# Optimization experiments

Hardware: AMD Instinct MI355X
Metric: run time of the kernel (lower is better)

## Reference

```python
import jax, jax.numpy as jnp
import numpy as np

N_NODES = 50000
N_EDGES = 500000
HIDDEN = 128
N_REL = 8


def setup_inputs() -> dict:
    key = jax.random.key(0)
    ks = jax.random.split(key, 6)
    node_states = jax.random.normal(ks[0], (N_NODES, HIDDEN), dtype=jnp.float32)
    edge_index = jax.random.randint(ks[1], (2, N_EDGES), 0, N_NODES, dtype=jnp.int64)
    edge_type = jax.random.randint(ks[2], (N_EDGES,), 0, N_REL, dtype=jnp.int64)
    # nn.Linear params: weight [out, in], applied as x @ W.T (+ b)
    W_self = jax.random.normal(ks[3], (HIDDEN, HIDDEN), dtype=jnp.float32) / np.sqrt(HIDDEN)
    b_self = jax.random.normal(ks[4], (HIDDEN,), dtype=jnp.float32) * 0.01
    W_rel = jax.random.normal(ks[5], (N_REL, HIDDEN, HIDDEN), dtype=jnp.float32) / np.sqrt(HIDDEN)
    return {"node_states": node_states, "edge_index": edge_index, "edge_type": edge_type,
            "W_self": W_self, "b_self": b_self, "W_rel": W_rel}


def reference(node_states, edge_index, edge_type, W_self, b_self, W_rel):
    # Per-relation gather -> linear -> scatter-add, with mean (degree) normalization.
    # Dropout is identity (eval mode).
    n_nodes = node_states.shape[0]
    n_rel = W_rel.shape[0]
    src = edge_index[0]
    dst = edge_index[1]
    xs = node_states[src]                                  # [E, d] gather once
    # Select per-edge relation transform without materializing [E, R, d]:
    # fixed small loop over relations, masked accumulate.
    messages = jnp.zeros_like(xs)
    for r in range(n_rel):
        m_r = xs @ W_rel[r].T                              # [E, d]
        messages = messages + jnp.where((edge_type == r)[:, None], m_r, 0.0)
    agg = jax.ops.segment_sum(messages, dst, num_segments=n_nodes)          # [N, d]
    deg = jax.ops.segment_sum(jnp.ones((dst.shape[0], 1), node_states.dtype),
                              dst, num_segments=n_nodes)                    # [N, 1]
    agg = agg / jnp.maximum(deg, 1.0)
    out = jax.nn.relu(node_states @ W_self.T + b_self + agg)
    return out
```

## Files before the change

kernel.cpp:

```cpp
#include <hip/hip_runtime.h>

#define HIDDEN 128
#define N_REL 8
#define ZCOLS 1152
#define BK 32
#define CPAD 136

typedef short short8 __attribute__((ext_vector_type(8)));
typedef float f32x4 __attribute__((ext_vector_type(4)));

__device__ inline float dot4f(float4 a, float4 b) {
  return a.x*b.x + a.y*b.y + a.z*b.z + a.w*b.w;
}

__device__ inline unsigned short f32_to_bf16(float f) {
  unsigned u = __float_as_uint(f);
  unsigned r = (u + 0x7FFFu + ((u >> 16) & 1u)) >> 16;
  return (unsigned short)r;
}

__device__ inline float bf16_to_f32(unsigned short h) {
  return __uint_as_float(((unsigned)h) << 16);
}

__device__ inline void gload_lds16(const unsigned short* g, unsigned short* l) {
  __builtin_amdgcn_global_load_lds(
      (const __attribute__((address_space(1))) void*)g,
      (__attribute__((address_space(3))) void*)l, 16, 0, 0);
}

__global__ void zero_i(int* __restrict__ p, int n) {
  int i = blockIdx.x * blockDim.x + threadIdx.x;
  int stride = gridDim.x * blockDim.x;
  for (; i < n; i += stride) p[i] = 0;
}

__global__ void hist_dst(const int* __restrict__ ei, int E, int* __restrict__ deg) {
  int i = blockIdx.x * blockDim.x + threadIdx.x;
  int stride = gridDim.x * blockDim.x;
  for (int e = i; e < E; e += stride) atomicAdd(&deg[ei[E + e]], 1);
}

__global__ void scan_pass1(const int* __restrict__ deg, int N, int N1,
                           int* __restrict__ rs, int* __restrict__ bsum) {
  __shared__ int sh[256];
  int tid = threadIdx.x;
  int i = blockIdx.x * 256 + tid;
  int v = (i < N) ? deg[i] : 0;
  sh[tid] = v;
  __syncthreads();
  for (int off = 1; off < 256; off <<= 1) {
    int x = (tid >= off) ? sh[tid - off] : 0;
    __syncthreads();
    sh[tid] += x;
    __syncthreads();
  }
  if (i < N1) rs[i] = sh[tid] - v;
  if (tid == 255) bsum[blockIdx.x] = sh[255];
}

__global__ void scan_pass2(int* __restrict__ bsum, int nb) {
  __shared__ int sh[256];
  int tid = threadIdx.x;
  int v = (tid < nb) ? bsum[tid] : 0;
  sh[tid] = v;
  __syncthreads();
  for (int off = 1; off < 256; off <<= 1) {
    int x = (tid >= off) ? sh[tid - off] : 0;
    __syncthreads();
    sh[tid] += x;
    __syncthreads();
  }
  if (tid < nb) bsum[tid] = sh[tid] - v;
}

__global__ void scan_pass3(int* __restrict__ rs, const int* __restrict__ bsum,
                           int* __restrict__ cursor, int N, int N1) {
  int i = blockIdx.x * 256 + threadIdx.x;
  if (i < N1) {
    int v = rs[i] + bsum[blockIdx.x];
    rs[i] = v;
    if (i < N) cursor[i] = v;
  }
}

__global__ void scatter_sorted(const int* __restrict__ ei, const int* __restrict__ et,
                               int E, int* __restrict__ cursor, int* __restrict__ sorted) {
  int i = blockIdx.x * blockDim.x + threadIdx.x;
  int stride = gridDim.x * blockDim.x;
  for (int e = i; e < E; e += stride) {
    int d = ei[E + e];
    int pos = atomicAdd(&cursor[d], 1);
    sorted[pos] = ei[e] | (et[e] << 24);
  }
}


__global__ void convert_xw(const float* __restrict__ ns,
                           const float* __restrict__ Ws, const float* __restrict__ Wr,
                           unsigned short* __restrict__ Xb,
                           unsigned short* __restrict__ Wb, int N) {
  int totalX = N * (HIDDEN / 8);
  int totalW = ZCOLS * (HIDDEN / 8);
  int i = blockIdx.x * blockDim.x + threadIdx.x;
  int stride = gridDim.x * blockDim.x;
  for (; i < totalX + totalW; i += stride) {
    const float* src;
    unsigned short* dst;
    if (i < totalX) {
      int row = i >> 4;
      int off = (i & 15) * 8;
      src = ns + (size_t)row * HIDDEN + off;
      dst = Xb + (size_t)row * HIDDEN + off;
    } else {
      int w = i - totalX;
      int j = w >> 4;
      int k = (w & 15) * 8;
      src = (j < HIDDEN) ? Ws + (size_t)j * HIDDEN + k
                         : Wr + (size_t)(j - HIDDEN) * HIDDEN + k;
      dst = Wb + (size_t)j * HIDDEN + k;
    }
    float4 a = *(const float4*)src, b = *(const float4*)(src + 4);
    ushort4 h0, h1;
    h0.x = f32_to_bf16(a.x); h0.y = f32_to_bf16(a.y);
    h0.z = f32_to_bf16(a.z); h0.w = f32_to_bf16(a.w);
    h1.x = f32_to_bf16(b.x); h1.y = f32_to_bf16(b.y);
    h1.z = f32_to_bf16(b.z); h1.w = f32_to_bf16(b.w);
    *(ushort4*)dst = h0;
    *(ushort4*)(dst + 4) = h1;
  }
}

__global__ __launch_bounds__(256) void gemm_z(
    const unsigned short* __restrict__ Xb, const unsigned short* __restrict__ Wb,
    unsigned short* __restrict__ Z, int N)
{
  __shared__ __align__(16) char smem[128 * CPAD * 2];
  unsigned short (*As)[128][BK] = (unsigned short (*)[128][BK])smem;
  unsigned short (*Bs)[128][BK] = (unsigned short (*)[128][BK])(smem + 16384);
  unsigned short (*Ct)[CPAD]    = (unsigned short (*)[CPAD])smem;

  int nwg = (int)gridDim.x;
  int orig = blockIdx.x;
  int q = nwg >> 3, r = nwg & 7;
  int xcd = orig & 7, off = orig >> 3;
  int bid = (xcd < r ? xcd * (q + 1) : r * (q + 1) + (xcd - r) * q) + off;

  int t = threadIdx.x;
  int lane = t & 63;
  int wave = t >> 6;
  int colb = lane & 15;
  int kq = (lane >> 4) * 8;
  int wr = (wave >> 1) * 64;
  int wc = (wave & 1) * 64;
  int rowbase = (bid / (ZCOLS / 128)) * 128;
  int colbase = (bid % (ZCOLS / 128)) * 128;

  int srow0 = t >> 2,         sk = (t & 3) * 8;
  int srow1 = (256 + t) >> 2;

  int ga0 = rowbase + srow0; if (ga0 >= N) ga0 = N - 1;
  int ga1 = rowbase + srow1; if (ga1 >= N) ga1 = N - 1;
  int gb0 = colbase + srow0; if (gb0 >= ZCOLS) gb0 = ZCOLS - 1;
  int gb1 = colbase + srow1; if (gb1 >= ZCOLS) gb1 = ZCOLS - 1;

  f32x4 acc[4][4];
  #pragma unroll
  for (int m = 0; m < 4; ++m)
    #pragma unroll
    for (int n = 0; n < 4; ++n) acc[m][n] = (f32x4){0.f, 0.f, 0.f, 0.f};

  gload_lds16(Xb + (size_t)ga0 * HIDDEN + sk, &As[0][srow0][sk]);
  gload_lds16(Xb + (size_t)ga1 * HIDDEN + sk, &As[0][srow1][sk]);
  gload_lds16(Wb + (size_t)gb0 * HIDDEN + sk, &Bs[0][srow0][sk]);
  gload_lds16(Wb + (size_t)gb1 * HIDDEN + sk, &Bs[0][srow1][sk]);
  __syncthreads();

  int cur = 0;
  for (int ks = 0; ks < 4; ++ks) {
    if (ks < 3) {
      int k0 = (ks + 1) * BK;
      gload_lds16(Xb + (size_t)ga0 * HIDDEN + k0 + sk, &As[cur ^ 1][srow0][sk]);
      gload_lds16(Xb + (size_t)ga1 * HIDDEN + k0 + sk, &As[cur ^ 1][srow1][sk]);
      gload_lds16(Wb + (size_t)gb0 * HIDDEN + k0 + sk, &Bs[cur ^ 1][srow0][sk]);
      gload_lds16(Wb + (size_t)gb1 * HIDDEN + k0 + sk, &Bs[cur ^ 1][srow1][sk]);
    }

    short8 a[4], bb[4];
    #pragma unroll
    for (int m = 0; m < 4; ++m)
      a[m] = *(const short8*)&As[cur][wr + m * 16 + colb][kq];
    #pragma unroll
    for (int n = 0; n < 4; ++n)
      bb[n] = *(const short8*)&Bs[cur][wc + n * 16 + colb][kq];

    #pragma unroll
    for (int m = 0; m < 4; ++m)
      #pragma unroll
      for (int n = 0; n < 4; ++n)
        acc[m][n] = __builtin_amdgcn_mfma_f32_16x16x32_bf16(a[m], bb[n],
                                                            acc[m][n], 0, 0, 0);
    if (ks < 3) {
      __syncthreads();
      cur ^= 1;
    }
  }

  __syncthreads();
  #pragma unroll
  for (int m = 0; m < 4; ++m) {
    int row = wr + m * 16 + (lane >> 4) * 4;
    #pragma unroll
    for (int n = 0; n < 4; ++n) {
      int c = wc + n * 16 + colb;
      #pragma unroll
      for (int rr = 0; rr < 4; ++rr)
        Ct[row + rr][c] = f32_to_bf16(acc[m][n][rr]);
    }
  }
  __syncthreads();

  int rowt = t >> 4;
  int ck = (t & 15) * 8;
  for (int p = 0; p < 8; ++p) {
    int row = p * 16 + rowt;
    int gr = rowbase + row;
    if (gr < N) {
      short8 v = *(const short8*)&Ct[row][ck];
      *(short8*)(Z + (size_t)gr * ZCOLS + colbase + ck) = v;
    }
  }
}

__global__ __launch_bounds__(256) void gather_out(
    const unsigned short* __restrict__ Z, const int* __restrict__ sorted,
    const int* __restrict__ rs, const float* __restrict__ b,
    float* __restrict__ out, int N)
{
  int wid = (int)((blockIdx.x * (unsigned)blockDim.x + threadIdx.x) >> 6);
  int lane = threadIdx.x & 63;
  if (wid >= N) return;
  int s0 = rs[wid], s1 = rs[wid + 1];

  int g = lane >> 3;
  int cl = lane & 7;

  float acc[16];
  #pragma unroll
  for (int k = 0; k < 16; ++k) acc[k] = 0.f;

  for (int eb = s0; eb < s1; eb += 64) {
    int m = min(64, s1 - eb);
    int sv = (lane < m) ? sorted[eb + lane] : 0;
    for (int j = 0; j < m; j += 8) {
      int e = j + g;
      int pk = __shfl(sv, e);
      if (e < m) {
        int src = pk & 0x00FFFFFF;
        if (src >= N) src = 0;
        int sl = (pk >> 24) & 7;
        const unsigned short* base = Z + (size_t)src * ZCOLS + HIDDEN + sl * HIDDEN;
        short8 v0 = *(const short8*)(base + cl * 8);
        short8 v1 = *(const short8*)(base + 64 + cl * 8);
        #pragma unroll
        for (int k = 0; k < 8; ++k) {
          acc[k]     += bf16_to_f32((unsigned short)v0[k]);
          acc[8 + k] += bf16_to_f32((unsigned short)v1[k]);
        }
      }
    }
  }

  #pragma unroll
  for (int k = 0; k < 16; ++k) {
    acc[k] += __shfl_xor(acc[k], 32);
    acc[k] += __shfl_xor(acc[k], 16);
    acc[k] += __shfl_xor(acc[k], 8);
  }

  if (g == 0) {
    float inv = (s1 > s0) ? 1.0f / (float)(s1 - s0) : 0.0f;
    const unsigned short* zp = Z + (size_t)wid * ZCOLS;
    short8 zv0 = *(const short8*)(zp + cl * 8);
    short8 zv1 = *(const short8*)(zp + 64 + cl * 8);
    float* op = out + (size_t)wid * HIDDEN;
    #pragma unroll
    for (int h = 0; h < 2; ++h) {
      const short8& zv = h ? zv1 : zv0;
      int cbase = h * 64 + cl * 8;
      float4 b0 = *(const float4*)(b + cbase);
      float4 b1 = *(const float4*)(b + cbase + 4);
      float4 o0, o1;
      o0.x = fmaxf(bf16_to_f32((unsigned short)zv[0]) + b0.x + acc[h * 8 + 0] * inv, 0.f);
      o0.y = fmaxf(bf16_to_f32((unsigned short)zv[1]) + b0.y + acc[h * 8 + 1] * inv, 0.f);
      o0.z = fmaxf(bf16_to_f32((unsigned short)zv[2]) + b0.z + acc[h * 8 + 2] * inv, 0.f);
      o0.w = fmaxf(bf16_to_f32((unsigned short)zv[3]) + b0.w + acc[h * 8 + 3] * inv, 0.f);
      o1.x = fmaxf(bf16_to_f32((unsigned short)zv[4]) + b1.x + acc[h * 8 + 4] * inv, 0.f);
      o1.y = fmaxf(bf16_to_f32((unsigned short)zv[5]) + b1.y + acc[h * 8 + 5] * inv, 0.f);
      o1.z = fmaxf(bf16_to_f32((unsigned short)zv[6]) + b1.z + acc[h * 8 + 6] * inv, 0.f);
      o1.w = fmaxf(bf16_to_f32((unsigned short)zv[7]) + b1.w + acc[h * 8 + 7] * inv, 0.f);
      *(float4*)(op + cbase) = o0;
      *(float4*)(op + cbase + 4) = o1;
    }
  }
}


__global__ __launch_bounds__(256) void gather_T_f32(
    const float* __restrict__ ns, const int* __restrict__ sorted,
    const int* __restrict__ rs, float* __restrict__ T, int N)
{
  int wid = (int)((blockIdx.x * (unsigned)blockDim.x + threadIdx.x) >> 6);
  int lane = threadIdx.x & 63;
  if (wid >= N) return;
  int s0 = rs[wid], s1 = rs[wid + 1];

  float2 acc[N_REL];
  #pragma unroll
  for (int r = 0; r < N_REL; ++r) { acc[r].x = 0.f; acc[r].y = 0.f; }

  for (int eb = s0; eb < s1; eb += 64) {
    int m = min(64, s1 - eb);
    int pk = (lane < m) ? sorted[eb + lane] : 0;
    for (int j = 0; j < m; ++j) {
      int pkj = __shfl(pk, j);
      int src = pkj & 0x00FFFFFF;
      int r = (pkj >> 24) & 7;
      float2 x = *(const float2*)(ns + (size_t)src * HIDDEN + lane * 2);
      #pragma unroll
      for (int rr = 0; rr < N_REL; ++rr)
        if (r == rr) { acc[rr].x += x.x; acc[rr].y += x.y; }
    }
  }

  float inv = (s1 > s0) ? 1.0f / (float)(s1 - s0) : 0.0f;
  float2* Tp = (float2*)(T + (size_t)wid * (N_REL * HIDDEN));
  #pragma unroll
  for (int r = 0; r < N_REL; ++r) {
    float2 o; o.x = acc[r].x * inv; o.y = acc[r].y * inv;
    Tp[r * 64 + lane] = o;
  }
}

__global__ __launch_bounds__(256) void out_kernel_f32(
    const float* __restrict__ ns, const float* __restrict__ T,
    const float* __restrict__ Ws, const float* __restrict__ Wrel,
    const float* __restrict__ b, float* __restrict__ out, int N)
{
  __shared__ float Xs[64][HIDDEN];
  int t = threadIdx.x;
  int base = blockIdx.x * 64;
  int cnt = min(64, N - base);
  int jg = t & 31;
  int eg = t >> 5;

  float acc[8][4];
  #pragma unroll
  for (int e = 0; e < 8; ++e)
    #pragma unroll
    for (int u = 0; u < 4; ++u) acc[e][u] = 0.f;

  for (int c = 0; c < 9; ++c) {
    for (int qq = t; qq < cnt * 32; qq += 256) {
      int e = qq >> 5, k4 = qq & 31;
      const float4* p = (c == 0)
          ? (const float4*)(ns + (size_t)(base + e) * HIDDEN)
          : (const float4*)(T + (size_t)(base + e) * (N_REL * HIDDEN) + (c - 1) * HIDDEN);
      ((float4*)Xs[e])[k4] = p[k4];
    }
    __syncthreads();

    const float* Wp = ((c == 0) ? Ws : (Wrel + (size_t)(c - 1) * HIDDEN * HIDDEN))
                      + (size_t)jg * 4 * HIDDEN;
    for (int kc = 0; kc < HIDDEN; kc += 8) {
      float4 wa[4], wb[4];
      #pragma unroll
      for (int u = 0; u < 4; ++u) {
        wa[u] = *(const float4*)(Wp + u * HIDDEN + kc);
        wb[u] = *(const float4*)(Wp + u * HIDDEN + kc + 4);
      }
      #pragma unroll
      for (int e = 0; e < 8; ++e) {
        float4 xa = ((const float4*)Xs[eg * 8 + e])[kc >> 2];
        float4 xb = ((const float4*)Xs[eg * 8 + e])[(kc >> 2) + 1];
        #pragma unroll
        for (int u = 0; u < 4; ++u)
          acc[e][u] += dot4f(xa, wa[u]) + dot4f(xb, wb[u]);
      }
    }
    __syncthreads();
  }

  float bj[4];
  *(float4*)bj = *(const float4*)(b + jg * 4);

  #pragma unroll
  for (int e = 0; e < 8; ++e) {
    int row = eg * 8 + e;
    if (row < cnt) {
      float4 o;
      o.x = fmaxf(acc[e][0] + bj[0], 0.f);
      o.y = fmaxf(acc[e][1] + bj[1], 0.f);
      o.z = fmaxf(acc[e][2] + bj[2], 0.f);
      o.w = fmaxf(acc[e][3] + bj[3], 0.f);
      *(float4*)(out + (size_t)(base + row) * HIDDEN + jg * 4) = o;
    }
  }
}


extern "C" void kernel_launch(void* const* d_in, const int* in_sizes, int n_in,
                              void* d_out, int out_size, void* d_ws, size_t ws_size,
                              hipStream_t stream) {
  const float* node_states = (const float*)d_in[0];
  const int*   edge_index  = (const int*)d_in[1];
  const int*   edge_type   = (const int*)d_in[2];
  const float* W_self      = (const float*)d_in[3];
  const float* b_self      = (const float*)d_in[4];
  const float* W_rel       = (const float*)d_in[5];
  float* out = (float*)d_out;

  const int E = in_sizes[2];
  const int N = in_sizes[0] / HIDDEN;
  const int N1 = N + 1;
  const int NB = (N1 + 255) / 256;

  const size_t ints_elems = (size_t)N + (size_t)N1 + (size_t)N + 256 + (size_t)E;

  const size_t xb_e = (size_t)N * HIDDEN;
  const size_t wb_e = (size_t)ZCOLS * HIDDEN;
  const size_t z_e  = (size_t)N * ZCOLS;
  const size_t needA = (xb_e + wb_e + z_e) * 2 + ints_elems * 4 + 64;

  const size_t needB = ((size_t)N * N_REL * HIDDEN + ints_elems) * 4 + 64;

  if (ws_size >= needA && NB <= 256 && N <= (1 << 24)) {
    unsigned short* Xb = (unsigned short*)d_ws;
    unsigned short* Wb = Xb + xb_e;
    unsigned short* Z  = Wb + wb_e;
    int* deg    = (int*)(Z + z_e);
    int* rs     = deg + N;
    int* cursor = rs + N1;
    int* bsum   = cursor + N;
    int* sorted = bsum + 256;

    zero_i<<<64, 256, 0, stream>>>(deg, N);
    hist_dst<<<1024, 256, 0, stream>>>(edge_index, E, deg);
    scan_pass1<<<NB, 256, 0, stream>>>(deg, N, N1, rs, bsum);
    scan_pass2<<<1, 256, 0, stream>>>(bsum, NB);
    scan_pass3<<<NB, 256, 0, stream>>>(rs, bsum, cursor, N, N1);
    scatter_sorted<<<1024, 256, 0, stream>>>(edge_index, edge_type, E, cursor, sorted);

    convert_xw<<<1024, 256, 0, stream>>>(node_states, W_self, W_rel, Xb, Wb, N);

    int zblocks = ((N + 127) / 128) * (ZCOLS / 128);
    gemm_z<<<zblocks, 256, 0, stream>>>(Xb, Wb, Z, N);
    gather_out<<<(N + 3) / 4, 256, 0, stream>>>(Z, sorted, rs, b_self, out, N);
  } else if (ws_size >= needB && NB <= 256 && N <= (1 << 24)) {
    float* T    = (float*)d_ws;
    int* deg    = (int*)(T + (size_t)N * N_REL * HIDDEN);
    int* rs     = deg + N;
    int* cursor = rs + N1;
    int* bsum   = cursor + N;
    int* sorted = bsum + 256;

    zero_i<<<64, 256, 0, stream>>>(deg, N);
    hist_dst<<<1024, 256, 0, stream>>>(edge_index, E, deg);
    scan_pass1<<<NB, 256, 0, stream>>>(deg, N, N1, rs, bsum);
    scan_pass2<<<1, 256, 0, stream>>>(bsum, NB);
    scan_pass3<<<NB, 256, 0, stream>>>(rs, bsum, cursor, N, N1);
    scatter_sorted<<<1024, 256, 0, stream>>>(edge_index, edge_type, E, cursor, sorted);

    gather_T_f32<<<(N + 3) / 4, 256, 0, stream>>>(node_states, sorted, rs, T, N);
    out_kernel_f32<<<(N + 63) / 64, 256, 0, stream>>>(node_states, T, W_self, W_rel,
                                                      b_self, out, N);
  }
}
```

Baseline: 131.2 us.

## Fuse fp32-to-bf16 node conversion into GEMM and keep full A row-block resident

The separate conversion of node_states to a bf16 buffer is removed. Each GEMM block now loads a 64-row fp32 slab of X once, converts it to bf16 in LDS, and loops over all nine 128-column output tiles while streaming only weight tiles through a double buffer. This drops the Xb write and re-read and shrinks the convert kernel to the weights alone. In exchange there are fewer, longer blocks (about 782), more barriers per block, and a smaller per-wave MFMA tile, which can lower occupancy and parallelism.

Measured after the change: 156.1 us. 1.19x slower.

```diff
diff --git a/kernel.cpp b/kernel.cpp
--- a/kernel.cpp
+++ b/kernel.cpp
@@ -4,7 +4,7 @@
 #define N_REL 8
 #define ZCOLS 1152
 #define BK 32
-#define CPAD 136
+#define APAD 136
 
 typedef short short8 __attribute__((ext_vector_type(8)));
 typedef float f32x4 __attribute__((ext_vector_type(4)));
@@ -96,138 +96,136 @@
 }
 
 
-__global__ void convert_xw(const float* __restrict__ ns,
-                           const float* __restrict__ Ws, const float* __restrict__ Wr,
-                           unsigned short* __restrict__ Xb,
-                           unsigned short* __restrict__ Wb, int N) {
-  int totalX = N * (HIDDEN / 8);
-  int totalW = ZCOLS * (HIDDEN / 8);
+__global__ void convert_w(const float* __restrict__ Ws, const float* __restrict__ Wr,
+                          unsigned short* __restrict__ Wb) {
   int i = blockIdx.x * blockDim.x + threadIdx.x;
+  int total = ZCOLS * (HIDDEN / 8);
   int stride = gridDim.x * blockDim.x;
-  for (; i < totalX + totalW; i += stride) {
-    const float* src;
-    unsigned short* dst;
-    if (i < totalX) {
-      int row = i >> 4;
-      int off = (i & 15) * 8;
-      src = ns + (size_t)row * HIDDEN + off;
-      dst = Xb + (size_t)row * HIDDEN + off;
-    } else {
-      int w = i - totalX;
-      int j = w >> 4;
-      int k = (w & 15) * 8;
-      src = (j < HIDDEN) ? Ws + (size_t)j * HIDDEN + k
-                         : Wr + (size_t)(j - HIDDEN) * HIDDEN + k;
-      dst = Wb + (size_t)j * HIDDEN + k;
-    }
+  for (; i < total; i += stride) {
+    int j = i >> 4;
+    int k = (i & 15) * 8;
+    const float* src = (j < HIDDEN)
+        ? Ws + (size_t)j * HIDDEN + k
+        : Wr + (size_t)(j - HIDDEN) * HIDDEN + k;
     float4 a = *(const float4*)src, b = *(const float4*)(src + 4);
     ushort4 h0, h1;
     h0.x = f32_to_bf16(a.x); h0.y = f32_to_bf16(a.y);
     h0.z = f32_to_bf16(a.z); h0.w = f32_to_bf16(a.w);
     h1.x = f32_to_bf16(b.x); h1.y = f32_to_bf16(b.y);
     h1.z = f32_to_bf16(b.z); h1.w = f32_to_bf16(b.w);
-    *(ushort4*)dst = h0;
-    *(ushort4*)(dst + 4) = h1;
+    unsigned short* q = Wb + (size_t)j * HIDDEN + k;
+    *(ushort4*)q = h0;
+    *(ushort4*)(q + 4) = h1;
   }
 }
 
 __global__ __launch_bounds__(256) void gemm_z(
-    const unsigned short* __restrict__ Xb, const unsigned short* __restrict__ Wb,
+    const float* __restrict__ X, const unsigned short* __restrict__ Wb,
     unsigned short* __restrict__ Z, int N)
 {
-  __shared__ __align__(16) char smem[128 * CPAD * 2];
-  unsigned short (*As)[128][BK] = (unsigned short (*)[128][BK])smem;
-  unsigned short (*Bs)[128][BK] = (unsigned short (*)[128][BK])(smem + 16384);
-  unsigned short (*Ct)[CPAD]    = (unsigned short (*)[CPAD])smem;
-
-  int nwg = (int)gridDim.x;
-  int orig = blockIdx.x;
-  int q = nwg >> 3, r = nwg & 7;
-  int xcd = orig & 7, off = orig >> 3;
-  int bid = (xcd < r ? xcd * (q + 1) : r * (q + 1) + (xcd - r) * q) + off;
+  __shared__ __align__(16) unsigned short As[64][APAD];
+  __shared__ __align__(16) unsigned short Bs[2][128][BK];
+  __shared__ __align__(16) unsigned short Ct[64][APAD];
 
   int t = threadIdx.x;
   int lane = t & 63;
   int wave = t >> 6;
   int colb = lane & 15;
-  int kq = (lane >> 4) * 8;
-  int wr = (wave >> 1) * 64;
+  int kgrp = lane >> 4;
+  int kq = kgrp * 8;
+  int wr = (wave >> 1) * 32;
   int wc = (wave & 1) * 64;
-  int rowbase = (bid / (ZCOLS / 128)) * 128;
-  int colbase = (bid % (ZCOLS / 128)) * 128;
-
-  int srow0 = t >> 2,         sk = (t & 3) * 8;
-  int srow1 = (256 + t) >> 2;
-
-  int ga0 = rowbase + srow0; if (ga0 >= N) ga0 = N - 1;
-  int ga1 = rowbase + srow1; if (ga1 >= N) ga1 = N - 1;
-  int gb0 = colbase + srow0; if (gb0 >= ZCOLS) gb0 = ZCOLS - 1;
-  int gb1 = colbase + srow1; if (gb1 >= ZCOLS) gb1 = ZCOLS - 1;
-
-  f32x4 acc[4][4];
-  #pragma unroll
-  for (int m = 0; m < 4; ++m)
+  int rowbase = blockIdx.x * 64;
+
+  {
+    int ar = t >> 2;
+    int ac = (t & 3) * 32;
+    int gr = rowbase + ar; if (gr >= N) gr = N - 1;
+    const float* src = X + (size_t)gr * HIDDEN + ac;
+    #pragma unroll
+    for (int u = 0; u < 4; ++u) {
+      float4 f0 = *(const float4*)(src + u * 8);
+      float4 f1 = *(const float4*)(src + u * 8 + 4);
+      short8 h;
+      h[0] = (short)f32_to_bf16(f0.x); h[1] = (short)f32_to_bf16(f0.y);
+      h[2] = (short)f32_to_bf16(f0.z); h[3] = (short)f32_to_bf16(f0.w);
+      h[4] = (short)f32_to_bf16(f1.x); h[5] = (short)f32_to_bf16(f1.y);
+      h[6] = (short)f32_to_bf16(f1.z); h[7] = (short)f32_to_bf16(f1.w);
+      *(short8*)&As[ar][ac + u * 8] = h;
+    }
+  }
+
+  int srow = t >> 2;
+  int sk = (t & 3) * 8;
+
+  gload_lds16(Wb + (size_t)srow * HIDDEN + sk, &Bs[0][srow][sk]);
+  gload_lds16(Wb + (size_t)(64 + srow) * HIDDEN + sk, &Bs[0][64 + srow][sk]);
+  __syncthreads();
+
+  f32x4 acc[2][4];
+  #pragma unroll
+  for (int m = 0; m < 2; ++m)
     #pragma unroll
     for (int n = 0; n < 4; ++n) acc[m][n] = (f32x4){0.f, 0.f, 0.f, 0.f};
 
-  gload_lds16(Xb + (size_t)ga0 * HIDDEN + sk, &As[0][srow0][sk]);
-  gload_lds16(Xb + (size_t)ga1 * HIDDEN + sk, &As[0][srow1][sk]);
-  gload_lds16(Wb + (size_t)gb0 * HIDDEN + sk, &Bs[0][srow0][sk]);
-  gload_lds16(Wb + (size_t)gb1 * HIDDEN + sk, &Bs[0][srow1][sk]);
-  __syncthreads();
-
-  int cur = 0;
-  for (int ks = 0; ks < 4; ++ks) {
-    if (ks < 3) {
-      int k0 = (ks + 1) * BK;
-      gload_lds16(Xb + (size_t)ga0 * HIDDEN + k0 + sk, &As[cur ^ 1][srow0][sk]);
-      gload_lds16(Xb + (size_t)ga1 * HIDDEN + k0 + sk, &As[cur ^ 1][srow1][sk]);
-      gload_lds16(Wb + (size_t)gb0 * HIDDEN + k0 + sk, &Bs[cur ^ 1][srow0][sk]);
-      gload_lds16(Wb + (size_t)gb1 * HIDDEN + k0 + sk, &Bs[cur ^ 1][srow1][sk]);
-    }
-
-    short8 a[4], bb[4];
-    #pragma unroll
-    for (int m = 0; m < 4; ++m)
-      a[m] = *(const short8*)&As[cur][wr + m * 16 + colb][kq];
+  for (int s = 0; s < 36; ++s) {
+    int ks = s & 3;
+    int cur = s & 1;
+    if (s < 35) {
+      int s2 = s + 1;
+      int ct2 = s2 >> 2, ks2 = s2 & 3;
+      const unsigned short* w0 =
+          Wb + (size_t)(ct2 * 128 + srow) * HIDDEN + ks2 * 32 + sk;
+      gload_lds16(w0, &Bs[cur ^ 1][srow][sk]);
+      gload_lds16(w0 + (size_t)64 * HIDDEN, &Bs[cur ^ 1][64 + srow][sk]);
+    }
+
+    short8 a[2], bb[4];
+    #pragma unroll
+    for (int m = 0; m < 2; ++m)
+      a[m] = *(const short8*)&As[wr + m * 16 + colb][ks * 32 + kq];
     #pragma unroll
     for (int n = 0; n < 4; ++n)
       bb[n] = *(const short8*)&Bs[cur][wc + n * 16 + colb][kq];
 
     #pragma unroll
-    for (int m = 0; m < 4; ++m)
+    for (int m = 0; m < 2; ++m)
       #pragma unroll
       for (int n = 0; n < 4; ++n)
         acc[m][n] = __builtin_amdgcn_mfma_f32_16x16x32_bf16(a[m], bb[n],
                                                             acc[m][n], 0, 0, 0);
-    if (ks < 3) {
+    __syncthreads();
+
+    if (ks == 3) {
+      int ct = s >> 2;
+      #pragma unroll
+      for (int m = 0; m < 2; ++m) {
+        int row = wr + m * 16 + kgrp * 4;
+        #pragma unroll
+        for (int n = 0; n < 4; ++n) {
+          int c = wc + n * 16 + colb;
+          #pragma unroll
+          for (int rr = 0; rr < 4; ++rr)
+            Ct[row + rr][c] = f32_to_bf16(acc[m][n][rr]);
+        }
+      }
       __syncthreads();
-      cur ^= 1;
-    }
-  }
-
-  __syncthreads();
-  #pragma unroll
-  for (int m = 0; m < 4; ++m) {
-    int row = wr + m * 16 + (lane >> 4) * 4;
-    #pragma unroll
-    for (int n = 0; n < 4; ++n) {
-      int c = wc + n * 16 + colb;
-      #pragma unroll
-      for (int rr = 0; rr < 4; ++rr)
-        Ct[row + rr][c] = f32_to_bf16(acc[m][n][rr]);
-    }
-  }
-  __syncthreads();
-
-  int rowt = t >> 4;
-  int ck = (t & 15) * 8;
-  for (int p = 0; p < 8; ++p) {
-    int row = p * 16 + rowt;
-    int gr = rowbase + row;
-    if (gr < N) {
-      short8 v = *(const short8*)&Ct[row][ck];
-      *(short8*)(Z + (size_t)gr * ZCOLS + colbase + ck) = v;
+      int rowt = t >> 4;
+      int ck = (t & 15) * 8;
+      #pragma unroll
+      for (int p = 0; p < 4; ++p) {
+        int row = p * 16 + rowt;
+        int gr = rowbase + row;
+        if (gr < N) {
+          short8 v = *(const short8*)&Ct[row][ck];
+          *(short8*)(Z + (size_t)gr * ZCOLS + ct * 128 + ck) = v;
+        }
+      }
+      __syncthreads();
+      #pragma unroll
+      for (int m = 0; m < 2; ++m)
+        #pragma unroll
+        for (int n = 0; n < 4; ++n) acc[m][n] = (f32x4){0.f, 0.f, 0.f, 0.f};
     }
   }
 }
@@ -427,16 +425,14 @@
 
   const size_t ints_elems = (size_t)N + (size_t)N1 + (size_t)N + 256 + (size_t)E;
 
-  const size_t xb_e = (size_t)N * HIDDEN;
   const size_t wb_e = (size_t)ZCOLS * HIDDEN;
   const size_t z_e  = (size_t)N * ZCOLS;
-  const size_t needA = (xb_e + wb_e + z_e) * 2 + ints_elems * 4 + 64;
+  const size_t needA = (wb_e + z_e) * 2 + ints_elems * 4 + 64;
 
   const size_t needB = ((size_t)N * N_REL * HIDDEN + ints_elems) * 4 + 64;
 
   if (ws_size >= needA && NB <= 256 && N <= (1 << 24)) {
-    unsigned short* Xb = (unsigned short*)d_ws;
-    unsigned short* Wb = Xb + xb_e;
+    unsigned short* Wb = (unsigned short*)d_ws;
     unsigned short* Z  = Wb + wb_e;
     int* deg    = (int*)(Z + z_e);
     int* rs     = deg + N;
@@ -451,10 +447,9 @@
     scan_pass3<<<NB, 256, 0, stream>>>(rs, bsum, cursor, N, N1);
     scatter_sorted<<<1024, 256, 0, stream>>>(edge_index, edge_type, E, cursor, sorted);
 
-    convert_xw<<<1024, 256, 0, stream>>>(node_states, W_self, W_rel, Xb, Wb, N);
-
-    int zblocks = ((N + 127) / 128) * (ZCOLS / 128);
-    gemm_z<<<zblocks, 256, 0, stream>>>(Xb, Wb, Z, N);
+    convert_w<<<72, 256, 0, stream>>>(W_self, W_rel, Wb);
+
+    gemm_z<<<(N + 63) / 64, 256, 0, stream>>>(node_states, Wb, Z, N);
     gather_out<<<(N + 3) / 4, 256, 0, stream>>>(Z, sorted, rs, b_self, out, N);
   } else if (ws_size >= needB && NB <= 256 && N <= (1 << 24)) {
     float* T    = (float*)d_ws;
```
